# Kernel tuning notes

Measured on AMD Instinct MI355X. Metric: run time of the kernel, lower is better.

The kernel has to match this reference:

```python
import jax, jax.numpy as jnp
import numpy as np

N = 20000      # nodes
E = 320000     # edges (avg degree 16)
C = 128        # channels (num_features from hidden_irreps 128x0e+128x1o)
R = 8          # radial basis size
S = 10         # num_species
H = 64         # radial MLP hidden
M = 16         # MLP_irreps = 16x0e
AVG_NEIGH = 16.0


def setup_inputs() -> dict:
    key = jax.random.key(0)
    ks = jax.random.split(key, 24)
    d = {}
    d["vectors"] = jax.random.normal(ks[0], (E, 3), jnp.float32)
    d["lengths"] = jax.random.uniform(ks[1], (E, 1), jnp.float32)
    d["node_feats"] = jax.random.normal(ks[2], (N, C), jnp.float32)
    species = jax.random.randint(ks[3], (N,), 0, S)
    d["node_attrs"] = jax.nn.one_hot(species, S, dtype=jnp.float32)
    d["edge_feats"] = jax.random.normal(ks[4], (E, R), jnp.float32)
    d["edge_index"] = jax.random.randint(ks[5], (2, E), 0, N)
    p = lambda k, shape, sc: jax.random.normal(k, shape, jnp.float32) * sc
    d["W_up"] = p(ks[6], (C, C), C ** -0.5)
    d["radial_w1"] = p(ks[7], (R + 1, H), (R + 1) ** -0.5)
    d["radial_b1"] = jnp.zeros((H,), jnp.float32)
    d["radial_w2"] = p(ks[8], (H, 2 * C), H ** -0.5)
    d["Wd0"] = p(ks[9], (C, C), C ** -0.5)
    d["Wd1"] = p(ks[10], (C, C), C ** -0.5)
    d["Wprod0"] = p(ks[11], (S, 5, C), 1.0)   # per-species symmetric-contraction weights, 0e paths
    d["Wprod1"] = p(ks[12], (S, 4, C), 1.0)   # per-species weights, 1o paths
    d["Wp0"] = p(ks[13], (C, C), C ** -0.5)
    d["Wp1"] = p(ks[14], (C, C), C ** -0.5)
    d["Wr1"] = p(ks[15], (C, M), C ** -0.5)
    d["Wr2"] = p(ks[16], (M, C), M ** -0.5)
    d["Wg"] = p(ks[17], (M, 1), M ** -0.5)
    d["wv"] = p(ks[18], (C, 1), C ** -0.5)
    return d


def _forward(vectors, lengths, node_feats, node_attrs, edge_feats,
             W_up, radial_w1, radial_b1, radial_w2, Wd0, Wd1,
             Wprod0, Wprod1, Wp0, Wp1, Wr1, Wr2, Wg, wv, edge_index):
    senders, receivers = edge_index[0], edge_index[1]
    # --- spherical harmonics (normalize=True), l=0 constant, l=1 ~ sqrt(3)*unit_vec ---
    u = vectors / (jnp.linalg.norm(vectors, axis=1, keepdims=True) + 1e-9)
    Y1 = jnp.sqrt(3.0) * u                                    # [E,3]
    # --- DiffusionInteractionBlock: linear up, radial-weighted tp conv, scatter, linear down ---
    h = node_feats @ W_up                                     # [N,C]
    hs = h[senders]                                           # [E,C] gather
    rad_in = jnp.concatenate([edge_feats, lengths], axis=1)   # [E,R+1]
    rad = jax.nn.silu(rad_in @ radial_w1 + radial_b1) @ radial_w2  # [E,2C]
    w0, w1 = rad[:, :C], rad[:, C:]
    m0 = w0 * hs                                              # [E,C]   0e x 0e -> 0e
    m1 = (w1 * hs)[:, None, :] * Y1[:, :, None]               # [E,3,C] 0e x 1o -> 1o
    s0 = jax.ops.segment_sum(m0, receivers, num_segments=N) / AVG_NEIGH
    s1 = jax.ops.segment_sum(m1, receivers, num_segments=N) / AVG_NEIGH
    a0 = s0 @ Wd0                                             # [N,C]
    a1 = s1 @ Wd1                                             # [N,3,C]
    # --- EquivariantProductBasisBlock: symmetric contraction, correlation=3, per-species weights ---
    dot11 = jnp.sum(a1 * a1, axis=1)                          # [N,C]  1o.1o -> 0e
    paths0 = jnp.stack([a0, a0 * a0, dot11, a0 ** 3, a0 * dot11], axis=1)          # [N,5,C]
    paths1 = jnp.stack([a1, a0[:, None, :] * a1, (a0 ** 2)[:, None, :] * a1,
                        dot11[:, None, :] * a1], axis=1)                            # [N,4,3,C]
    b0 = jnp.einsum('ns,spc,npc->nc', node_attrs, Wprod0, paths0)
    b1 = jnp.einsum('ns,spc,npic->nic', node_attrs, Wprod1, paths1)
    h0 = b0 @ Wp0                                             # [N,C]
    h1 = b1 @ Wp1                                             # [N,3,C]
    # --- NonLinearReadoutBlock: gated MLP readout ---
    mh = jax.nn.silu(h0 @ Wr1)                                # [N,M]
    scalars = mh @ Wr2                                        # [N,C]
    gate = jax.nn.silu(mh @ Wg)                               # [N,1]
    vec = (h1 @ wv)[..., 0] * gate                            # [N,3]
    nf = jnp.concatenate([h0, h1.reshape(N, 3 * C)], axis=1)  # [N,4C]
    return scalars, vec, nf


def reference(vectors, lengths, node_feats, node_attrs, edge_feats, edge_index,
              W_up, radial_w1, radial_b1, radial_w2, Wd0, Wd1,
              Wprod0, Wprod1, Wp0, Wp1, Wr1, Wr2, Wg, wv):
    # returns (node_out[:, :-3], node_out[:, -3:], node_feats)
    return _forward(vectors, lengths, node_feats, node_attrs, edge_feats,
                    W_up, radial_w1, radial_b1, radial_w2, Wd0, Wd1,
                    Wprod0, Wprod1, Wp0, Wp1, Wr1, Wr2, Wg, wv, edge_index)
```

## Files before the change

### kernel.cpp

```cpp
#include <hip/hip_runtime.h>

#define NN 20000
#define NE 320000
#define CC 128
#define SS 10
#define NWIN 10000

typedef __attribute__((ext_vector_type(8))) short short8;
typedef __attribute__((ext_vector_type(4))) float f32x4;

#define MFMA16(a, b, c) __builtin_amdgcn_mfma_f32_16x16x32_bf16(a, b, c, 0, 0, 0)

__device__ __forceinline__ float silu_f(float x) { return x / (1.f + __expf(-x)); }

__device__ __forceinline__ unsigned short f2bf(float x) {
  unsigned u = __float_as_uint(x);
  unsigned r = u + 0x7FFFu + ((u >> 16) & 1u);
  return (unsigned short)(r >> 16);
}
__device__ __forceinline__ float bf2f(unsigned short h) {
  return __uint_as_float(((unsigned)h) << 16);
}
__device__ __forceinline__ void cvt8(const float* xs, short8& ah, short8& al) {
#pragma unroll
  for (int j = 0; j < 8; ++j) {
    const unsigned short h = f2bf(xs[j]);
    ah[j] = (short)h;
    al[j] = (short)f2bf(xs[j] - bf2f(h));
  }
}

__global__ __launch_bounds__(256) void k_prep_w2(const float* __restrict__ W2,
                                                 const float* __restrict__ W1,
                                                 unsigned short* __restrict__ w2h,
                                                 unsigned short* __restrict__ w2l,
                                                 unsigned short* __restrict__ w1ph,
                                                 unsigned short* __restrict__ w1pl) {
  const int i = blockIdx.x * 256 + threadIdx.x;
  if (i < 64 * 256) {
    const int col = i % 256, k = i / 256;
    const float x = W2[i];
    const unsigned short h = f2bf(x);
    w2h[col * 64 + k] = h;
    w2l[col * 64 + k] = f2bf(x - bf2f(h));
  }
  if (i < 2048) {
    const int col = i >> 5, k = i & 31;
    const float x = (k < 9) ? W1[k * 64 + col] : 0.f;
    const unsigned short h = f2bf(x);
    w1ph[col * 32 + k] = h;
    w1pl[col * 32 + k] = f2bf(x - bf2f(h));
  }
}

__global__ __launch_bounds__(256) void k_prep_w128(
    const float* __restrict__ Wd0, const float* __restrict__ Wd1,
    const float* __restrict__ Wp0, const float* __restrict__ Wp1,
    unsigned short* __restrict__ wh, unsigned short* __restrict__ wl) {
  const int b = blockIdx.x;
  const int m = b >> 6;
  const int i = (b & 63) * 256 + threadIdx.x;
  const float* W = (m == 0) ? Wd0 : (m == 1) ? Wd1 : (m == 2) ? Wp0 : Wp1;
  const int k = i >> 7, col = i & 127;
  const float x = W[i];
  const unsigned short h = f2bf(x);
  wh[m * 16384 + col * 128 + k] = h;
  wl[m * 16384 + col * 128 + k] = f2bf(x - bf2f(h));
}

__global__ __launch_bounds__(128) void k_node_h(const float* __restrict__ nf,
                                                const float* __restrict__ W,
                                                float* __restrict__ h) {
  __shared__ __align__(16) float rows[8][CC];
  const int c = threadIdx.x;
  const int n0 = blockIdx.x * 8;
#pragma unroll
  for (int q = 0; q < 8; ++q) rows[q][c] = nf[(n0 + q) * CC + c];
  __syncthreads();
  float acc[8] = {0.f, 0.f, 0.f, 0.f, 0.f, 0.f, 0.f, 0.f};
  for (int k = 0; k < CC; k += 4) {
    const float w0 = W[(k + 0) * CC + c];
    const float w1 = W[(k + 1) * CC + c];
    const float w2 = W[(k + 2) * CC + c];
    const float w3 = W[(k + 3) * CC + c];
#pragma unroll
    for (int q = 0; q < 8; ++q) {
      float4 v = *(const float4*)&rows[q][k];
      acc[q] += v.x * w0 + v.y * w1 + v.z * w2 + v.w * w3;
    }
  }
#pragma unroll
  for (int q = 0; q < 8; ++q) h[(n0 + q) * CC + c] = acc[q];
}

__global__ void k_hist(const int* __restrict__ recv, int* __restrict__ cnt) {
  int i = blockIdx.x * blockDim.x + threadIdx.x;
  if (i < NE) atomicAdd(&cnt[recv[i]], 1);
}

__global__ __launch_bounds__(1024) void k_scan2(int* cntcur, int* offs) {
  const int t = threadIdx.x;
  int v[20];
  int tot = 0;
  if (t < 1000) {
#pragma unroll
    for (int i = 0; i < 20; ++i) {
      v[i] = cntcur[t * 20 + i];
      tot += v[i];
    }
  }
  const int lane = t & 63;
  int x = tot;
#pragma unroll
  for (int off = 1; off < 64; off <<= 1) {
    int y = __shfl_up(x, off, 64);
    if (lane >= off) x += y;
  }
  __shared__ int wt[16], wo[16];
  if (lane == 63) wt[t >> 6] = x;
  __syncthreads();
  if (t == 0) {
    int a = 0;
    for (int w = 0; w < 16; ++w) {
      wo[w] = a;
      a += wt[w];
    }
    offs[NN] = a;
  }
  __syncthreads();
  int run = wo[t >> 6] + x - tot;
  if (t < 1000) {
#pragma unroll
    for (int i = 0; i < 20; ++i) {
      offs[t * 20 + i] = run;
      cntcur[t * 20 + i] = run;
      run += v[i];
    }
  }
}

__global__ void k_fill2(const int* __restrict__ recv, const int* __restrict__ snd,
                        const float* __restrict__ vectors,
                        const float* __restrict__ lengths,
                        const float* __restrict__ efeat, int* __restrict__ cur,
                        float* __restrict__ edata) {
  int i = blockIdx.x * blockDim.x + threadIdx.x;
  if (i < NE) {
    const int r = recv[i];
    const int pos = atomicAdd(&cur[r], 1);
    const float vx = vectors[i * 3 + 0];
    const float vy = vectors[i * 3 + 1];
    const float vz = vectors[i * 3 + 2];
    const float nr = sqrtf(vx * vx + vy * vy + vz * vz) + 1e-9f;
    const float sc = 1.7320508075688772f / nr;
    float4 a = {vx * sc, vy * sc, vz * sc, lengths[i]};
    float4 b = *(const float4*)&efeat[(size_t)i * 8];
    float4 c = *(const float4*)&efeat[(size_t)i * 8 + 4];
    float4 d;
    ((int*)&d)[0] = snd[i];
    d.y = 0.f; d.z = 0.f; d.w = 0.f;
    float* rec = edata + (size_t)pos * 16;
    *(float4*)rec = a;
    *(float4*)(rec + 4) = b;
    *(float4*)(rec + 8) = c;
    *(float4*)(rec + 12) = d;
  }
}

__global__ __launch_bounds__(256) void k_edge5(
    const float* __restrict__ hbuf, const float* __restrict__ B1,
    const unsigned short* __restrict__ w2h, const unsigned short* __restrict__ w2l,
    const unsigned short* __restrict__ w1ph, const unsigned short* __restrict__ w1pl,
    const int* __restrict__ offs, const float* __restrict__ edata,
    float* __restrict__ sout) {
  __shared__ __align__(16) float ed[2][64][20];
  __shared__ __align__(16) unsigned short hidh[64][72];
  __shared__ __align__(16) unsigned short hidl[64][72];
  __shared__ __align__(16) unsigned short w1hs[64 * 36];
  __shared__ __align__(16) unsigned short w1ls[64 * 36];

  const int t = threadIdx.x;
  const int l = t & 63, wv = t >> 6, lg = l >> 4, lm = l & 15;
  const int half = wv & 1;
  const bool isw1 = wv >= 2;

  for (int i = t; i < 2048; i += 256) {
    const int col = i >> 5, k = i & 31;
    w1hs[col * 36 + k] = w1ph[i];
    w1ls[col * 36 + k] = w1pl[i];
  }

  short8 Bh[4][2], Bl[4][2];
#pragma unroll
  for (int ct = 0; ct < 4; ++ct)
#pragma unroll
    for (int s = 0; s < 2; ++s) {
      const int col = wv * 64 + ct * 16 + lm;
      Bh[ct][s] = *(const short8*)&w2h[col * 64 + s * 32 + lg * 8];
      Bl[ct][s] = *(const short8*)&w2l[col * 64 + s * 32 + lg * 8];
    }
  float b1r[4];
#pragma unroll
  for (int ct = 0; ct < 4; ++ct) b1r[ct] = B1[ct * 16 + lm];

  const int nb = blockIdx.x * 2;
  const int o0 = offs[nb], o1 = offs[nb + 1], o2 = offs[nb + 2];

  float p0[2][4] = {};
  float px[2][4] = {}, py[2][4] = {}, pz[2][4] = {};

  const int se = t >> 2, sq = t & 3;

  float4 sreg = {0.f, 0.f, 0.f, 0.f};
  {
    const int idx = o0 + se;
    if (idx < o2) sreg = *(const float4*)&edata[(size_t)idx * 16 + sq * 4];
    *(float4*)&ed[0][se][sq * 4] = sreg;
    sreg = (float4){0.f, 0.f, 0.f, 0.f};
    const int idx1 = o0 + 64 + se;
    if (idx1 < o2) sreg = *(const float4*)&edata[(size_t)idx1 * 16 + sq * 4];
  }
  __syncthreads();

#define CONSUME(GR, ACC, HC, YA, YB, YC)                                       \
  do {                                                                         \
    float vvv[4][4];                                                           \
    _Pragma("unroll") for (int ct = 0; ct < 4; ++ct)                           \
        _Pragma("unroll") for (int r = 0; r < 4; ++r)                          \
            vvv[ct][r] = (ACC)[ct][r] * (HC)[ct][r];                           \
    const bool fast0 = ((GR) + 16 <= o1);                                      \
    const bool fast1 = ((GR) >= o1) && ((GR) + 16 <= o2);                      \
    if (fast0) {                                                               \
      if (!isw1) {                                                             \
        _Pragma("unroll") for (int ct = 0; ct < 4; ++ct)                       \
            _Pragma("unroll") for (int r = 0; r < 4; ++r)                      \
                p0[0][ct] += vvv[ct][r];                                       \
      } else {                                                                 \
        _Pragma("unroll") for (int ct = 0; ct < 4; ++ct)                       \
            _Pragma("unroll") for (int r = 0; r < 4; ++r) {                    \
          px[0][ct] += vvv[ct][r] * (YA)[r];                                   \
          py[0][ct] += vvv[ct][r] * (YB)[r];                                   \
          pz[0][ct] += vvv[ct][r] * (YC)[r];                                   \
        }                                                                      \
      }                                                                        \
    } else if (fast1) {                                                        \
      if (!isw1) {                                                             \
        _Pragma("unroll") for (int ct = 0; ct < 4; ++ct)                       \
            _Pragma("unroll") for (int r = 0; r < 4; ++r)                      \
                p0[1][ct] += vvv[ct][r];                                       \
      } else {                                                                 \
        _Pragma("unroll") for (int ct = 0; ct < 4; ++ct)                       \
            _Pragma("unroll") for (int r = 0; r < 4; ++r) {                    \
          px[1][ct] += vvv[ct][r] * (YA)[r];                                   \
          py[1][ct] += vvv[ct][r] * (YB)[r];                                   \
          pz[1][ct] += vvv[ct][r] * (YC)[r];                                   \
        }                                                                      \
      }                                                                        \
    } else {                                                                   \
      const int grow0 = (GR) + lg * 4;                                         \
      _Pragma("unroll") for (int sl = 0; sl < 2; ++sl) {                       \
        const int slo = sl ? o1 : o0;                                          \
        const int shi = sl ? o2 : o1;                                          \
        if (shi > (GR) && slo < (GR) + 16) {                                   \
          if (!isw1) {                                                         \
            _Pragma("unroll") for (int r = 0; r < 4; ++r) {                    \
              const bool in = (grow0 + r >= slo) && (grow0 + r < shi);         \
              _Pragma("unroll") for (int ct = 0; ct < 4; ++ct)                 \
                  p0[sl][ct] += in ? vvv[ct][r] : 0.f;                         \
            }                                                                  \
          } else {                                                             \
            _Pragma("unroll") for (int r = 0; r < 4; ++r) {                    \
              const bool in = (grow0 + r >= slo) && (grow0 + r < shi);         \
              _Pragma("unroll") for (int ct = 0; ct < 4; ++ct) {               \
                const float m = in ? vvv[ct][r] : 0.f;                         \
                px[sl][ct] += m * (YA)[r];                                     \
                py[sl][ct] += m * (YB)[r];                                     \
                pz[sl][ct] += m * (YC)[r];                                     \
              }                                                                \
            }                                                                  \
          }                                                                    \
        }                                                                      \
      }                                                                        \
    }                                                                          \
  } while (0)

  const int npass = (o2 - o0 + 63) >> 6;
  for (int p = 0; p < npass; ++p) {
    const int pb = p & 1;
    const int base = o0 + p * 64;
    {
      const int erow = wv * 16 + lm;
      short8 Ahi = (short8){0, 0, 0, 0, 0, 0, 0, 0};
      short8 Alo = (short8){0, 0, 0, 0, 0, 0, 0, 0};
      if (lg == 0) {
        const float4 e0 = *(const float4*)&ed[pb][erow][4];
        const float4 e1 = *(const float4*)&ed[pb][erow][8];
        float xs[8] = {e0.x, e0.y, e0.z, e0.w, e1.x, e1.y, e1.z, e1.w};
        cvt8(xs, Ahi, Alo);
      } else if (lg == 1) {
        const float ln = ed[pb][erow][3];
        const unsigned short h = f2bf(ln);
        Ahi[0] = (short)h;
        Alo[0] = (short)f2bf(ln - bf2f(h));
      }
      f32x4 ha[4];
#pragma unroll
      for (int ct = 0; ct < 4; ++ct) {
        const int col = ct * 16 + lm;
        const short8 wh = *(const short8*)&w1hs[col * 36 + lg * 8];
        const short8 wl = *(const short8*)&w1ls[col * 36 + lg * 8];
        f32x4 a = {0.f, 0.f, 0.f, 0.f};
        a = MFMA16(Ahi, wh, a);
        a = MFMA16(Ahi, wl, a);
        a = MFMA16(Alo, wh, a);
        ha[ct] = a;
      }
#pragma unroll
      for (int ct = 0; ct < 4; ++ct) {
        const int col = ct * 16 + lm;
#pragma unroll
        for (int r = 0; r < 4; ++r) {
          const float v = silu_f(ha[ct][r] + b1r[ct]);
          const int row = wv * 16 + lg * 4 + r;
          const unsigned short h = f2bf(v);
          hidh[row][col] = h;
          hidl[row][col] = f2bf(v - bf2f(h));
        }
      }
    }
    __syncthreads();
    {
      *(float4*)&ed[pb ^ 1][se][sq * 4] = sreg;
      sreg = (float4){0.f, 0.f, 0.f, 0.f};
      const int idx2 = base + 128 + se;
      if (idx2 < o2) sreg = *(const float4*)&edata[(size_t)idx2 * 16 + sq * 4];
    }
#pragma unroll 1
    for (int sp = 0; sp < 2; ++sp) {
      const int rb = sp * 32;
      const int gr0 = base + rb;
      if (gr0 >= o2) break;
      int sd0[4];
      float ya0[4], yb0[4], yc0[4];
#pragma unroll
      for (int r = 0; r < 4; ++r) {
        const int row = rb + lg * 4 + r;
        sd0[r] = __float_as_int(ed[pb][row][12]);
        ya0[r] = ed[pb][row][0];
        yb0[r] = ed[pb][row][1];
        yc0[r] = ed[pb][row][2];
      }
      float hc0[4][4];
#pragma unroll
      for (int ct = 0; ct < 4; ++ct) {
        const int col = half * 64 + ct * 16 + lm;
#pragma unroll
        for (int r = 0; r < 4; ++r) hc0[ct][r] = hbuf[(size_t)sd0[r] * CC + col];
      }
      short8 Ah0 = *(const short8*)&hidh[rb + lm][lg * 8];
      short8 Ah1 = *(const short8*)&hidh[rb + lm][32 + lg * 8];
      short8 Al0 = *(const short8*)&hidl[rb + lm][lg * 8];
      short8 Al1 = *(const short8*)&hidl[rb + lm][32 + lg * 8];
      f32x4 acc0[4];
#pragma unroll
      for (int ct = 0; ct < 4; ++ct) {
        f32x4 a = {0.f, 0.f, 0.f, 0.f};
        a = MFMA16(Ah0, Bh[ct][0], a);
        a = MFMA16(Ah0, Bl[ct][0], a);
        a = MFMA16(Al0, Bh[ct][0], a);
        a = MFMA16(Ah1, Bh[ct][1], a);
        a = MFMA16(Ah1, Bl[ct][1], a);
        a = MFMA16(Al1, Bh[ct][1], a);
        acc0[ct] = a;
      }
      const bool live1 = (gr0 + 16) < o2;
      if (live1) {
        int sd1[4];
        float ya1[4], yb1[4], yc1[4];
#pragma unroll
        for (int r = 0; r < 4; ++r) {
          const int row = rb + 16 + lg * 4 + r;
          sd1[r] = __float_as_int(ed[pb][row][12]);
          ya1[r] = ed[pb][row][0];
          yb1[r] = ed[pb][row][1];
          yc1[r] = ed[pb][row][2];
        }
        float hc1[4][4];
#pragma unroll
        for (int ct = 0; ct < 4; ++ct) {
          const int col = half * 64 + ct * 16 + lm;
#pragma unroll
          for (int r = 0; r < 4; ++r) hc1[ct][r] = hbuf[(size_t)sd1[r] * CC + col];
        }
        CONSUME(gr0, acc0, hc0, ya0, yb0, yc0);
        short8 Bh0_ = *(const short8*)&hidh[rb + 16 + lm][lg * 8];
        short8 Bh1_ = *(const short8*)&hidh[rb + 16 + lm][32 + lg * 8];
        short8 Bl0_ = *(const short8*)&hidl[rb + 16 + lm][lg * 8];
        short8 Bl1_ = *(const short8*)&hidl[rb + 16 + lm][32 + lg * 8];
        f32x4 acc1[4];
#pragma unroll
        for (int ct = 0; ct < 4; ++ct) {
          f32x4 a = {0.f, 0.f, 0.f, 0.f};
          a = MFMA16(Bh0_, Bh[ct][0], a);
          a = MFMA16(Bh0_, Bl[ct][0], a);
          a = MFMA16(Bl0_, Bh[ct][0], a);
          a = MFMA16(Bh1_, Bh[ct][1], a);
          a = MFMA16(Bh1_, Bl[ct][1], a);
          a = MFMA16(Bl1_, Bh[ct][1], a);
          acc1[ct] = a;
        }
        CONSUME(gr0 + 16, acc1, hc1, ya1, yb1, yc1);
      } else {
        CONSUME(gr0, acc0, hc0, ya0, yb0, yc0);
      }
    }
    __syncthreads();
  }
#undef CONSUME

  const float inv = 1.f / 16.f;
#pragma unroll
  for (int sl = 0; sl < 2; ++sl) {
    const int n = nb + sl;
    if (!isw1) {
#pragma unroll
      for (int ct = 0; ct < 4; ++ct) {
        float v = p0[sl][ct];
        v += __shfl_xor(v, 16, 64);
        v += __shfl_xor(v, 32, 64);
        if (lg == 0) sout[(size_t)n * 512 + half * 64 + ct * 16 + lm] = v * inv;
      }
    } else {
#pragma unroll
      for (int ct = 0; ct < 4; ++ct) {
        float vx = px[sl][ct], vy = py[sl][ct], vz = pz[sl][ct];
        vx += __shfl_xor(vx, 16, 64); vx += __shfl_xor(vx, 32, 64);
        vy += __shfl_xor(vy, 16, 64); vy += __shfl_xor(vy, 32, 64);
        vz += __shfl_xor(vz, 16, 64); vz += __shfl_xor(vz, 32, 64);
        if (lg == 0) {
          const int c = half * 64 + ct * 16 + lm;
          sout[(size_t)n * 512 + 128 + c] = vx * inv;
          sout[(size_t)n * 512 + 256 + c] = vy * inv;
          sout[(size_t)n * 512 + 384 + c] = vz * inv;
        }
      }
    }
  }
}

__global__ __launch_bounds__(256, 2) void k_down3(
    const float* __restrict__ sbuf, const float* __restrict__ attrs,
    const unsigned short* __restrict__ wbh, const unsigned short* __restrict__ wbl,
    const float* __restrict__ Wprod0, const float* __restrict__ Wprod1,
    const float* __restrict__ Wr1, const float* __restrict__ Wr2,
    const float* __restrict__ Wg, const float* __restrict__ wvv,
    float* __restrict__ out_scalars, float* __restrict__ out_vec,
    float* __restrict__ out_nf) {
  __shared__ __align__(16) char smem[35840];
  __shared__ int sidx_s[16];
  __shared__ float mh_s[16][17];
  __shared__ float gate_s[16];
  unsigned short* bh = (unsigned short*)smem;
  unsigned short* bl = bh + 8960;
  float* hX = (float*)smem;

  const int t = threadIdx.x;
  const int l = t & 63, wv = t >> 6, lg = l >> 4, lm = l & 15;
  const int n0 = blockIdx.x * 16;

  if (t < 16) {
    int si = 0;
#pragma unroll
    for (int s = 0; s < SS; ++s)
      si = (attrs[(size_t)(n0 + t) * SS + s] > 0.5f) ? s : si;
    sidx_s[t] = si;
  }

  short8 Wfh[2][2][4], Wfl[2][2][4];
#pragma unroll
  for (int mat = 0; mat < 2; ++mat)
#pragma unroll
    for (int ct = 0; ct < 2; ++ct)
#pragma unroll
      for (int ks = 0; ks < 4; ++ks) {
        const size_t off =
            (size_t)mat * 16384 + (size_t)(wv * 32 + ct * 16 + lm) * 128 + ks * 32 + lg * 8;
        Wfh[mat][ct][ks] = *(const short8*)&wbh[off];
        Wfl[mat][ct][ks] = *(const short8*)&wbl[off];
      }

  f32x4 acc[4][2];
#pragma unroll 1
  for (int comp = 0; comp < 4; ++comp) {
    short8 Ah[4], Al[4];
#pragma unroll
    for (int ks = 0; ks < 4; ++ks) {
      const size_t so = (size_t)(n0 + lm) * 512 + comp * 128 + ks * 32 + lg * 8;
      const float4 xa = *(const float4*)&sbuf[so];
      const float4 xb = *(const float4*)&sbuf[so + 4];
      float xs[8] = {xa.x, xa.y, xa.z, xa.w, xb.x, xb.y, xb.z, xb.w};
      cvt8(xs, Ah[ks], Al[ks]);
    }
    const int mat = comp ? 1 : 0;
#pragma unroll
    for (int ct = 0; ct < 2; ++ct) {
      f32x4 a = {0.f, 0.f, 0.f, 0.f};
#pragma unroll
      for (int ks = 0; ks < 4; ++ks) {
        a = MFMA16(Ah[ks], Wfh[mat][ct][ks], a);
        a = MFMA16(Ah[ks], Wfl[mat][ct][ks], a);
        a = MFMA16(Al[ks], Wfh[mat][ct][ks], a);
      }
      acc[comp][ct] = a;
    }
  }

#pragma unroll
  for (int ct = 0; ct < 2; ++ct) {
#pragma unroll
    for (int r = 0; r < 4; ++r) {
      const int node = lg * 4 + r;
      const int c = wv * 32 + ct * 16 + lm;
      const int si = sidx_s[node];
      const float a0 = acc[0][ct][r];
      const float ax = acc[1][ct][r], ay = acc[2][ct][r], az = acc[3][ct][r];
      const float dot = ax * ax + ay * ay + az * az;
      const float a2 = a0 * a0;
      const float* w0 = Wprod0 + (size_t)si * 5 * CC;
      const float* w1 = Wprod1 + (size_t)si * 4 * CC;
      const float b0v = w0[c] * a0 + w0[CC + c] * a2 + w0[2 * CC + c] * dot +
                        w0[3 * CC + c] * (a2 * a0) + w0[4 * CC + c] * (a0 * dot);
      const float fac =
          w1[c] + w1[CC + c] * a0 + w1[2 * CC + c] * a2 + w1[3 * CC + c] * dot;
      const float bv[4] = {b0v, ax * fac, ay * fac, az * fac};
#pragma unroll
      for (int m = 0; m < 4; ++m) {
        const int idx = (m * 16 + node) * 140 + c;
        const unsigned short h = f2bf(bv[m]);
        bh[idx] = h;
        bl[idx] = f2bf(bv[m] - bf2f(h));
      }
    }
  }

#pragma unroll
  for (int mat = 0; mat < 2; ++mat)
#pragma unroll
    for (int ct = 0; ct < 2; ++ct)
#pragma unroll
      for (int ks = 0; ks < 4; ++ks) {
        const size_t off = (size_t)(2 + mat) * 16384 +
                           (size_t)(wv * 32 + ct * 16 + lm) * 128 + ks * 32 + lg * 8;
        Wfh[mat][ct][ks] = *(const short8*)&wbh[off];
        Wfl[mat][ct][ks] = *(const short8*)&wbl[off];
      }
  __syncthreads();

  f32x4 acch[4][2];
#pragma unroll 1
  for (int comp = 0; comp < 4; ++comp) {
    short8 Ah[4], Al[4];
#pragma unroll
    for (int ks = 0; ks < 4; ++ks) {
      const int idx = (comp * 16 + lm) * 140 + ks * 32 + lg * 8;
      Ah[ks] = *(const short8*)&bh[idx];
      Al[ks] = *(const short8*)&bl[idx];
    }
    const int mat = comp ? 1 : 0;
#pragma unroll
    for (int ct = 0; ct < 2; ++ct) {
      f32x4 a = {0.f, 0.f, 0.f, 0.f};
#pragma unroll
      for (int ks = 0; ks < 4; ++ks) {
        a = MFMA16(Ah[ks], Wfh[mat][ct][ks], a);
        a = MFMA16(Ah[ks], Wfl[mat][ct][ks], a);
        a = MFMA16(Al[ks], Wfh[mat][ct][ks], a);
      }
      acch[comp][ct] = a;
    }
  }
  __syncthreads();

#pragma unroll
  for (int comp = 0; comp < 4; ++comp)
#pragma unroll
    for (int ct = 0; ct < 2; ++ct)
#pragma unroll
      for (int r = 0; r < 4; ++r) {
        const int node = lg * 4 + r;
        const int c = wv * 32 + ct * 16 + lm;
        hX[(comp * 16 + node) * 132 + c] = acch[comp][ct][r];
        out_nf[(size_t)(n0 + node) * 512 + comp * 128 + c] = acch[comp][ct][r];
      }
  __syncthreads();

  {
    const int node = t >> 4, m = t & 15;
    float a = 0.f;
    const float* Xn = &hX[node * 132];
    for (int k = 0; k < CC; k += 4) {
      const float4 h4 = *(const float4*)&Xn[k];
      a += h4.x * Wr1[(k + 0) * 16 + m] + h4.y * Wr1[(k + 1) * 16 + m] +
           h4.z * Wr1[(k + 2) * 16 + m] + h4.w * Wr1[(k + 3) * 16 + m];
    }
    mh_s[node][m] = silu_f(a);
  }
  __syncthreads();
  if (t < 16) {
    float g = 0.f;
#pragma unroll
    for (int m = 0; m < 16; ++m) g += mh_s[t][m] * Wg[m];
    gate_s[t] = silu_f(g);
  }
  __syncthreads();
  {
    const int node = t >> 4, cb = (t & 15) * 8;
#pragma unroll
    for (int j = 0; j < 8; ++j) {
      float a = 0.f;
#pragma unroll
      for (int m = 0; m < 16; ++m) a += mh_s[node][m] * Wr2[m * CC + cb + j];
      out_scalars[(size_t)(n0 + node) * CC + cb + j] = a;
    }
  }
  if (t < 48) {
    const int node = t / 3, i = t % 3;
    float a = 0.f;
    const float* Xn = &hX[((1 + i) * 16 + node) * 132];
    for (int k = 0; k < CC; k += 4) {
      const float4 h4 = *(const float4*)&Xn[k];
      const float4 w4 = *(const float4*)&wvv[k];
      a += h4.x * w4.x + h4.y * w4.y + h4.z * w4.z + h4.w * w4.w;
    }
    out_vec[(size_t)(n0 + node) * 3 + i] = a * gate_s[node];
  }
}

extern "C" void kernel_launch(void* const* d_in, const int* in_sizes, int n_in,
                              void* d_out, int out_size, void* d_ws, size_t ws_size,
                              hipStream_t stream) {
  const float* vectors    = (const float*)d_in[0];
  const float* lengths    = (const float*)d_in[1];
  const float* node_feats = (const float*)d_in[2];
  const float* node_attrs = (const float*)d_in[3];
  const float* edge_feats = (const float*)d_in[4];
  const int*   edge_index = (const int*)d_in[5];
  const float* W_up       = (const float*)d_in[6];
  const float* radial_w1  = (const float*)d_in[7];
  const float* radial_b1  = (const float*)d_in[8];
  const float* radial_w2  = (const float*)d_in[9];
  const float* Wd0        = (const float*)d_in[10];
  const float* Wd1        = (const float*)d_in[11];
  const float* Wprod0     = (const float*)d_in[12];
  const float* Wprod1     = (const float*)d_in[13];
  const float* Wp0        = (const float*)d_in[14];
  const float* Wp1        = (const float*)d_in[15];
  const float* Wr1        = (const float*)d_in[16];
  const float* Wr2        = (const float*)d_in[17];
  const float* Wg         = (const float*)d_in[18];
  const float* wv         = (const float*)d_in[19];

  float* out = (float*)d_out;
  float* out_scalars = out;
  float* out_vec = out + (size_t)NN * CC;
  float* out_nf = out + (size_t)NN * CC + (size_t)NN * 3;
  float* sbuf = out_nf;
  float* hbuf = out_scalars;

  int* cnt = (int*)d_ws;
  int* offs = cnt + NN;
  float* edata = (float*)(offs + NN + 4);
  unsigned short* w2h = (unsigned short*)(edata + (size_t)NE * 16);
  unsigned short* w2l = w2h + 16384;
  unsigned short* w1ph = w2l + 16384;
  unsigned short* w1pl = w1ph + 2048;
  unsigned short* wbh = w1pl + 2048;
  unsigned short* wbl = wbh + 4 * 16384;

  const int* senders = edge_index;
  const int* receivers = edge_index + NE;

  hipMemsetAsync(cnt, 0, NN * sizeof(int), stream);
  k_prep_w2<<<64, 256, 0, stream>>>(radial_w2, radial_w1, w2h, w2l, w1ph, w1pl);
  k_prep_w128<<<256, 256, 0, stream>>>(Wd0, Wd1, Wp0, Wp1, wbh, wbl);
  k_node_h<<<NN / 8, 128, 0, stream>>>(node_feats, W_up, hbuf);
  k_hist<<<NE / 256, 256, 0, stream>>>(receivers, cnt);
  k_scan2<<<1, 1024, 0, stream>>>(cnt, offs);
  k_fill2<<<NE / 256, 256, 0, stream>>>(receivers, senders, vectors, lengths,
                                        edge_feats, cnt, edata);
  k_edge5<<<NWIN, 256, 0, stream>>>(hbuf, radial_b1, w2h, w2l, w1ph, w1pl,
                                    offs, edata, sbuf);
  k_down3<<<NN / 16, 256, 0, stream>>>(sbuf, node_attrs, wbh, wbl, Wprod0,
                                       Wprod1, Wr1, Wr2, Wg, wv,
                                       out_scalars, out_vec, out_nf);
}
```

Before: 355.8 us.

## Stage sender features in LDS via coalesced loads; keep W1 in registers

In the edge kernel, each thread now loads a contiguous 128-byte chunk of its edge's sender row of hbuf into registers as float4s at the start of every pass, before the radial MLP. After the MLP it stores them into a new shared tile, and the consume phase reads the features from LDS instead of issuing scattered per-element global gathers. The first-layer radial weights are also held in registers rather than staged through shared memory. The aim is coalesced, earlier-issued gathers that overlap with the MLP compute. The cost is a roughly 33 KB shared buffer and 32 extra live registers per thread, which may reduce occupancy.

```diff
diff --git a/kernel.cpp b/kernel.cpp
--- a/kernel.cpp
+++ b/kernel.cpp
@@ -167,7 +167,7 @@
   }
 }
 
-__global__ __launch_bounds__(256) void k_edge5(
+__global__ __launch_bounds__(256) void k_edge6(
     const float* __restrict__ hbuf, const float* __restrict__ B1,
     const unsigned short* __restrict__ w2h, const unsigned short* __restrict__ w2l,
     const unsigned short* __restrict__ w1ph, const unsigned short* __restrict__ w1pl,
@@ -176,20 +176,13 @@
   __shared__ __align__(16) float ed[2][64][20];
   __shared__ __align__(16) unsigned short hidh[64][72];
   __shared__ __align__(16) unsigned short hidl[64][72];
-  __shared__ __align__(16) unsigned short w1hs[64 * 36];
-  __shared__ __align__(16) unsigned short w1ls[64 * 36];
+  __shared__ __align__(16) float hlds[64 * 132];
 
   const int t = threadIdx.x;
   const int l = t & 63, wv = t >> 6, lg = l >> 4, lm = l & 15;
   const int half = wv & 1;
   const bool isw1 = wv >= 2;
 
-  for (int i = t; i < 2048; i += 256) {
-    const int col = i >> 5, k = i & 31;
-    w1hs[col * 36 + k] = w1ph[i];
-    w1ls[col * 36 + k] = w1pl[i];
-  }
-
   short8 Bh[4][2], Bl[4][2];
 #pragma unroll
   for (int ct = 0; ct < 4; ++ct)
@@ -199,6 +192,13 @@
       Bh[ct][s] = *(const short8*)&w2h[col * 64 + s * 32 + lg * 8];
       Bl[ct][s] = *(const short8*)&w2l[col * 64 + s * 32 + lg * 8];
     }
+  short8 W1h[4], W1l[4];
+#pragma unroll
+  for (int ct = 0; ct < 4; ++ct) {
+    const int col = ct * 16 + lm;
+    W1h[ct] = *(const short8*)&w1ph[col * 32 + lg * 8];
+    W1l[ct] = *(const short8*)&w1pl[col * 32 + lg * 8];
+  }
   float b1r[4];
 #pragma unroll
   for (int ct = 0; ct < 4; ++ct) b1r[ct] = B1[ct * 16 + lm];
@@ -288,6 +288,13 @@
   for (int p = 0; p < npass; ++p) {
     const int pb = p & 1;
     const int base = o0 + p * 64;
+    float4 hreg[8];
+    {
+      const int sd_st = __float_as_int(ed[pb][se][12]);
+      const float* hrow = &hbuf[(size_t)sd_st * CC + sq * 32];
+#pragma unroll
+      for (int j = 0; j < 8; ++j) hreg[j] = *(const float4*)&hrow[j * 4];
+    }
     {
       const int erow = wv * 16 + lm;
       short8 Ahi = (short8){0, 0, 0, 0, 0, 0, 0, 0};
@@ -306,13 +313,10 @@
       f32x4 ha[4];
 #pragma unroll
       for (int ct = 0; ct < 4; ++ct) {
-        const int col = ct * 16 + lm;
-        const short8 wh = *(const short8*)&w1hs[col * 36 + lg * 8];
-        const short8 wl = *(const short8*)&w1ls[col * 36 + lg * 8];
         f32x4 a = {0.f, 0.f, 0.f, 0.f};
-        a = MFMA16(Ahi, wh, a);
-        a = MFMA16(Ahi, wl, a);
-        a = MFMA16(Alo, wh, a);
+        a = MFMA16(Ahi, W1h[ct], a);
+        a = MFMA16(Ahi, W1l[ct], a);
+        a = MFMA16(Alo, W1h[ct], a);
         ha[ct] = a;
       }
 #pragma unroll
@@ -328,6 +332,11 @@
         }
       }
     }
+    {
+      float* hrow = &hlds[se * 132 + sq * 32];
+#pragma unroll
+      for (int j = 0; j < 8; ++j) *(float4*)&hrow[j * 4] = hreg[j];
+    }
     __syncthreads();
     {
       *(float4*)&ed[pb ^ 1][se][sq * 4] = sreg;
@@ -340,22 +349,20 @@
       const int rb = sp * 32;
       const int gr0 = base + rb;
       if (gr0 >= o2) break;
-      int sd0[4];
       float ya0[4], yb0[4], yc0[4];
 #pragma unroll
       for (int r = 0; r < 4; ++r) {
         const int row = rb + lg * 4 + r;
-        sd0[r] = __float_as_int(ed[pb][row][12]);
         ya0[r] = ed[pb][row][0];
         yb0[r] = ed[pb][row][1];
         yc0[r] = ed[pb][row][2];
       }
       float hc0[4][4];
 #pragma unroll
-      for (int ct = 0; ct < 4; ++ct) {
-        const int col = half * 64 + ct * 16 + lm;
-#pragma unroll
-        for (int r = 0; r < 4; ++r) hc0[ct][r] = hbuf[(size_t)sd0[r] * CC + col];
+      for (int r = 0; r < 4; ++r) {
+        const float* hb = &hlds[(rb + lg * 4 + r) * 132 + half * 64 + lm];
+#pragma unroll
+        for (int ct = 0; ct < 4; ++ct) hc0[ct][r] = hb[ct * 16];
       }
       short8 Ah0 = *(const short8*)&hidh[rb + lm][lg * 8];
       short8 Ah1 = *(const short8*)&hidh[rb + lm][32 + lg * 8];
@@ -375,22 +382,20 @@
       }
       const bool live1 = (gr0 + 16) < o2;
       if (live1) {
-        int sd1[4];
         float ya1[4], yb1[4], yc1[4];
 #pragma unroll
         for (int r = 0; r < 4; ++r) {
           const int row = rb + 16 + lg * 4 + r;
-          sd1[r] = __float_as_int(ed[pb][row][12]);
           ya1[r] = ed[pb][row][0];
           yb1[r] = ed[pb][row][1];
           yc1[r] = ed[pb][row][2];
         }
         float hc1[4][4];
 #pragma unroll
-        for (int ct = 0; ct < 4; ++ct) {
-          const int col = half * 64 + ct * 16 + lm;
-#pragma unroll
-          for (int r = 0; r < 4; ++r) hc1[ct][r] = hbuf[(size_t)sd1[r] * CC + col];
+        for (int r = 0; r < 4; ++r) {
+          const float* hb = &hlds[(rb + 16 + lg * 4 + r) * 132 + half * 64 + lm];
+#pragma unroll
+          for (int ct = 0; ct < 4; ++ct) hc1[ct][r] = hb[ct * 16];
         }
         CONSUME(gr0, acc0, hc0, ya0, yb0, yc0);
         short8 Bh0_ = *(const short8*)&hidh[rb + 16 + lm][lg * 8];
@@ -688,7 +693,7 @@
   k_scan2<<<1, 1024, 0, stream>>>(cnt, offs);
   k_fill2<<<NE / 256, 256, 0, stream>>>(receivers, senders, vectors, lengths,
                                         edge_feats, cnt, edata);
-  k_edge5<<<NWIN, 256, 0, stream>>>(hbuf, radial_b1, w2h, w2l, w1ph, w1pl,
+  k_edge6<<<NWIN, 256, 0, stream>>>(hbuf, radial_b1, w2h, w2l, w1ph, w1pl,
                                     offs, edata, sbuf);
   k_down3<<<NN / 16, 256, 0, stream>>>(sbuf, node_attrs, wbh, wbl, Wprod0,
                                        Wprod1, Wr1, Wr2, Wg, wv,
```

Measured after the change: 500.4 us. +40.6%, slower.
